# Performance work log

Hardware: AMD Instinct MI355X
Metric: run time of the kernel (lower is better)

Reference implementation:

```python
import jax, jax.numpy as jnp
import numpy as np

N_NODES = 100000
N_EDGES = 1600000
IN_DIM = 256
HIDDEN = 64


def setup_inputs() -> dict:
    key = jax.random.key(0)
    k0, k1, k2, k3 = jax.random.split(key, 4)
    x = jax.random.normal(k0, (N_NODES, IN_DIM), dtype=jnp.float32)
    edge_index = jax.random.randint(k1, (2, N_EDGES), 0, N_NODES, dtype=jnp.int64)
    # GCNConv weight [in_dim, hidden] + bias, MLP Linear(hidden, 1) + bias
    W = jax.random.normal(k2, (IN_DIM, HIDDEN), dtype=jnp.float32) * 0.05
    b = jnp.zeros((HIDDEN,), dtype=jnp.float32)
    w2 = jax.random.normal(k3, (HIDDEN, 1), dtype=jnp.float32) * 0.05
    b2 = jnp.zeros((1,), dtype=jnp.float32)
    return {"x": x, "edge_index": edge_index, "W": W, "b": b, "w2": w2, "b2": b2}


def reference(x, edge_index, W, b, w2, b2):
    N = x.shape[0]
    # PyG GCNConv default: add self-loops, symmetric normalization D^-1/2 A D^-1/2
    loops = jnp.arange(N, dtype=edge_index.dtype)
    src = jnp.concatenate([edge_index[0], loops])  # [E + N]
    dst = jnp.concatenate([edge_index[1], loops])
    h = x @ W  # [N, H] transform first (hidden < in_dim)
    deg = jax.ops.segment_sum(jnp.ones_like(dst, dtype=h.dtype), dst, num_segments=N)
    dinv = jnp.where(deg > 0, jax.lax.rsqrt(deg), 0.0)
    norm = dinv[src] * dinv[dst]  # [E + N]
    agg = jax.ops.segment_sum(h[src] * norm[:, None], dst, num_segments=N) + b  # [N, H]
    score = jax.nn.sigmoid(agg @ w2 + b2)  # [N, 1]
    return score.squeeze(-1)
```

## Files before the change

kernel.cpp:

```cpp
#include <hip/hip_runtime.h>
#include <math.h>

#define N_NODES 100000
#define N_EDGES 1600000
#define IN_DIM  256
#define HIDDEN  64

#define NB      32
#define EPB     50000
#define QPB     12500
#define SR      8
#define SRANGE  12544
#define PD      8
#define DNR     12800
#define DW      3200
#define DEGB    256

__global__ void __launch_bounds__(1024) fusedA_kernel(const float* __restrict__ x,
                                                      const float* __restrict__ W,
                                                      const float* __restrict__ w2,
                                                      const int4* __restrict__ dst4,
                                                      unsigned* __restrict__ partialD,
                                                      float* __restrict__ s) {
    __shared__ __align__(16) unsigned sh[DW];
    const int bid = blockIdx.x;
    if (bid < DEGB) {
        const int r  = bid & (PD - 1);
        const int bb = bid >> 3;
        const int nbase = r * DNR;
        for (int i = threadIdx.x; i < DW; i += 1024) sh[i] = 0u;
        __syncthreads();
        const int q0 = bb * QPB;
        for (int k = threadIdx.x; k < QPB; k += 1024) {
            int4 d4 = dst4[q0 + k];
            int d0 = d4.x - nbase, d1 = d4.y - nbase, d2 = d4.z - nbase, d3 = d4.w - nbase;
            if ((unsigned)d0 < (unsigned)DNR) atomicAdd(&sh[d0 >> 2], 1u << ((d0 & 3) * 8));
            if ((unsigned)d1 < (unsigned)DNR) atomicAdd(&sh[d1 >> 2], 1u << ((d1 & 3) * 8));
            if ((unsigned)d2 < (unsigned)DNR) atomicAdd(&sh[d2 >> 2], 1u << ((d2 & 3) * 8));
            if ((unsigned)d3 < (unsigned)DNR) atomicAdd(&sh[d3 >> 2], 1u << ((d3 & 3) * 8));
        }
        __syncthreads();
        unsigned* outp = partialD + (size_t)bid * DW;
        for (int i = threadIdx.x; i < DW; i += 1024) outp[i] = sh[i];
    } else {
        float* vsh = (float*)sh;
        if (threadIdx.x < IN_DIM) {
            const float4* wr  = (const float4*)(W + threadIdx.x * HIDDEN);
            const float4* w2r = (const float4*)w2;
            float acc = 0.f;
            #pragma unroll
            for (int j = 0; j < HIDDEN / 4; ++j) {
                float4 a = wr[j], q = w2r[j];
                acc += a.x * q.x + a.y * q.y + a.z * q.z + a.w * q.w;
            }
            vsh[threadIdx.x] = acc;
        }
        __syncthreads();
        const int wid  = threadIdx.x >> 6;
        const int lane = threadIdx.x & 63;
        const int gw   = (bid - DEGB) * 16 + wid;
        float4 vv = ((const float4*)vsh)[lane];
        for (int n = gw; n < N_NODES; n += 4096) {
            const float4* xr = (const float4*)(x + (size_t)n * IN_DIM);
            float4 a = xr[lane];
            float d = a.x * vv.x + a.y * vv.y + a.z * vv.z + a.w * vv.w;
            #pragma unroll
            for (int off = 32; off > 0; off >>= 1) d += __shfl_down(d, off, 64);
            if (lane == 0) s[n] = d;
        }
    }
}

__global__ void deg_merge_kernel(const unsigned* __restrict__ partialD,
                                 const float* __restrict__ s,
                                 float* __restrict__ dinv, float* __restrict__ t) {
    int w = blockIdx.x * blockDim.x + threadIdx.x;
    if (w >= N_NODES / 4) return;
    const int r = w / DW, j = w - r * DW;
    unsigned a0 = 0, a1 = 0, a2 = 0, a3 = 0;
    #pragma unroll 8
    for (int b = 0; b < NB; ++b) {
        unsigned p = partialD[(size_t)(b * PD + r) * DW + j];
        a0 += p & 255u; a1 += (p >> 8) & 255u; a2 += (p >> 16) & 255u; a3 += p >> 24;
    }
    const int n0 = w * 4;
    float4 sv = *(const float4*)(s + n0);
    float4 di, tv;
    di.x = rsqrtf((float)(a0 + 1)); di.y = rsqrtf((float)(a1 + 1));
    di.z = rsqrtf((float)(a2 + 1)); di.w = rsqrtf((float)(a3 + 1));
    tv.x = di.x * sv.x; tv.y = di.y * sv.y; tv.z = di.z * sv.z; tv.w = di.w * sv.w;
    *(float4*)(dinv + n0) = di;
    *(float4*)(t + n0) = tv;
}

__global__ void __launch_bounds__(1024) scat_hist_kernel(const int4* __restrict__ src4,
                                                         const int4* __restrict__ dst4,
                                                         const float* __restrict__ t,
                                                         float* __restrict__ partialU) {
    __shared__ float acc[SRANGE];
    const int r  = blockIdx.x & (SR - 1);
    const int bb = blockIdx.x >> 3;
    const int nbase = r * SRANGE;
    for (int i = threadIdx.x; i < SRANGE; i += 1024) acc[i] = 0.f;
    __syncthreads();
    const int q0 = bb * QPB;
    for (int k = threadIdx.x; k < QPB; k += 1024) {
        int4 d4 = dst4[q0 + k];
        int4 s4 = src4[q0 + k];
        int d0 = d4.x - nbase, d1 = d4.y - nbase, d2 = d4.z - nbase, d3 = d4.w - nbase;
        if ((unsigned)d0 < (unsigned)SRANGE) atomicAdd(&acc[d0], t[s4.x]);
        if ((unsigned)d1 < (unsigned)SRANGE) atomicAdd(&acc[d1], t[s4.y]);
        if ((unsigned)d2 < (unsigned)SRANGE) atomicAdd(&acc[d2], t[s4.z]);
        if ((unsigned)d3 < (unsigned)SRANGE) atomicAdd(&acc[d3], t[s4.w]);
    }
    __syncthreads();
    float* outp = partialU + (size_t)blockIdx.x * SRANGE;
    for (int i = threadIdx.x; i < SRANGE; i += 1024) outp[i] = acc[i];
}

__global__ void merge_final_kernel(const float* __restrict__ partialU,
                                   const float* __restrict__ dinv,
                                   const float* __restrict__ s,
                                   const float* __restrict__ b,
                                   const float* __restrict__ w2,
                                   const float* __restrict__ b2,
                                   float* __restrict__ out) {
    float c = b2[0];
    #pragma unroll 8
    for (int j = 0; j < HIDDEN; ++j) c += b[j] * w2[j];
    int n = blockIdx.x * blockDim.x + threadIdx.x;
    if (n >= N_NODES) return;
    const int r = n / SRANGE, j = n - r * SRANGE;
    float u = 0.f;
    #pragma unroll 8
    for (int bl = 0; bl < NB; ++bl)
        u += partialU[(size_t)(bl * SR + r) * SRANGE + j];
    float di = dinv[n];
    float pre = di * (u + di * s[n]) + c;
    out[n] = 1.f / (1.f + expf(-pre));
}

__global__ void wv_kernel(const float* __restrict__ W, const float* __restrict__ b,
                          const float* __restrict__ w2, const float* __restrict__ b2,
                          float* __restrict__ v, float* __restrict__ c) {
    int i = threadIdx.x;
    float acc = 0.f;
    for (int j = 0; j < HIDDEN; ++j) acc += W[i * HIDDEN + j] * w2[j];
    v[i] = acc;
    if (i == 0) {
        float cc = b2[0];
        for (int j = 0; j < HIDDEN; ++j) cc += b[j] * w2[j];
        *c = cc;
    }
}
__global__ void s_kernel(const float* __restrict__ x, const float* __restrict__ v,
                         float* __restrict__ s) {
    const int wave = threadIdx.x >> 6;
    const int lane = threadIdx.x & 63;
    const int n = blockIdx.x * 4 + wave;
    const float4* xr = (const float4*)(x + (size_t)n * IN_DIM);
    const float4* vr = (const float4*)v;
    float4 a  = xr[lane];
    float4 vv = vr[lane];
    float d = a.x * vv.x + a.y * vv.y + a.z * vv.z + a.w * vv.w;
    #pragma unroll
    for (int off = 32; off > 0; off >>= 1) d += __shfl_down(d, off, 64);
    if (lane == 0) s[n] = d;
}
__global__ void deg_kernel(const int* __restrict__ dst, int* __restrict__ cnt) {
    int e = blockIdx.x * blockDim.x + threadIdx.x;
    if (e < N_EDGES) atomicAdd(&cnt[dst[e]], 1);
}
__global__ void dinv_kernel(const int* __restrict__ cnt, const float* __restrict__ s,
                            float* __restrict__ dinv, float* __restrict__ t) {
    int n = blockIdx.x * blockDim.x + threadIdx.x;
    if (n < N_NODES) {
        float di = rsqrtf((float)(cnt[n] + 1));
        dinv[n] = di;
        t[n] = di * s[n];
    }
}
__global__ void scatter_kernel(const int* __restrict__ src, const int* __restrict__ dst,
                               const float* __restrict__ t, float* __restrict__ u) {
    int e = blockIdx.x * blockDim.x + threadIdx.x;
    if (e < N_EDGES) atomicAdd(&u[dst[e]], t[src[e]]);
}
__global__ void final_kernel(const float* __restrict__ dinv, const float* __restrict__ u,
                             const float* __restrict__ s, const float* __restrict__ c,
                             float* __restrict__ out) {
    int n = blockIdx.x * blockDim.x + threadIdx.x;
    if (n < N_NODES) {
        float di = dinv[n];
        float pre = di * (u[n] + di * s[n]) + c[0];
        out[n] = 1.f / (1.f + expf(-pre));
    }
}

extern "C" void kernel_launch(void* const* d_in, const int* in_sizes, int n_in,
                              void* d_out, int out_size, void* d_ws, size_t ws_size,
                              hipStream_t stream) {
    const float* x   = (const float*)d_in[0];
    const int*   ei  = (const int*)  d_in[1];
    const float* W   = (const float*)d_in[2];
    const float* b   = (const float*)d_in[3];
    const float* w2  = (const float*)d_in[4];
    const float* b2  = (const float*)d_in[5];
    float* out = (float*)d_out;

    const int* src = ei;
    const int* dst = ei + N_EDGES;

    float* ws   = (float*)d_ws;
    float*    v        = ws + 0;
    float*    c        = ws + 256;
    float*    s        = ws + 512;
    float*    t        = ws + 100608;
    float*    dinv     = ws + 200704;
    unsigned* partialD = (unsigned*)(ws + 300800);
    float*    partialU = ws + 1120000;
    const size_t need_bytes = (size_t)(1120000 + 256 * SRANGE) * 4;

    if (ws_size >= need_bytes) {
        fusedA_kernel<<<DEGB + 256, 1024, 0, stream>>>(x, W, w2, (const int4*)dst, partialD, s);
        deg_merge_kernel<<<(N_NODES / 4 + 255) / 256, 256, 0, stream>>>(partialD, s, dinv, t);
        scat_hist_kernel<<<NB * SR, 1024, 0, stream>>>((const int4*)src, (const int4*)dst, t, partialU);
        merge_final_kernel<<<(N_NODES + 511) / 512, 512, 0, stream>>>(partialU, dinv, s, b, w2, b2, out);
    } else {
        float* u   = ws + 300800;
        int*   cnt = (int*)(ws + 400800);
        hipMemsetAsync((char*)d_ws + (size_t)300800 * 4, 0, (size_t)200000 * 4, stream);
        wv_kernel<<<1, 256, 0, stream>>>(W, b, w2, b2, v, c);
        s_kernel<<<N_NODES / 4, 256, 0, stream>>>(x, v, s);
        deg_kernel<<<(N_EDGES + 255) / 256, 256, 0, stream>>>(dst, cnt);
        dinv_kernel<<<(N_NODES + 255) / 256, 256, 0, stream>>>(cnt, s, dinv, t);
        scatter_kernel<<<(N_EDGES + 255) / 256, 256, 0, stream>>>(src, dst, t, u);
        final_kernel<<<(N_NODES + 255) / 256, 256, 0, stream>>>(dinv, u, s, c, out);
    }
}
```

Before: 207.2 us.

## Fuse all stages into one cooperative kernel with grid-wide syncs

Replaces the four-kernel pipeline (degree histogram plus score GEMV, degree merge, scatter histogram, merge and final sigmoid) with a single cooperative kernel of 512 blocks. Stages are separated by grid.sync. The scatter stage is also re-split into 64 edge chunks by 8 node ranges. The goal is to remove kernel launch gaps and tail effects between the dependent stages. The cost is three grid-wide barriers, a larger partialU buffer, and lower parallelism in some stages. If the workspace is too small or the cooperative launch fails, it falls back to the old path. The old non-histogram fallback path is removed.

```diff
diff --git a/kernel.cpp b/kernel.cpp
--- a/kernel.cpp
+++ b/kernel.cpp
@@ -1,10 +1,151 @@
 #include <hip/hip_runtime.h>
+#include <hip/hip_cooperative_groups.h>
 #include <math.h>
+
+namespace cg = cooperative_groups;
 
 #define N_NODES 100000
 #define N_EDGES 1600000
 #define IN_DIM  256
 #define HIDDEN  64
+
+#define GRID    512
+#define TPB     512
+#define D_NB    32
+#define D_EPB   50000
+#define D_QPB   12500
+#define D_PD    8
+#define D_DNR   12800
+#define D_DW    3200
+#define S_NB    64
+#define S_EPB   25000
+#define S_QPB   6250
+#define S_SR    8
+#define S_RANGE 12544
+
+__global__ void __launch_bounds__(TPB, 4) mega_kernel(
+    const float* __restrict__ x, const float* __restrict__ W,
+    const float* __restrict__ b, const float* __restrict__ w2,
+    const float* __restrict__ b2,
+    const int4* __restrict__ src4, const int4* __restrict__ dst4,
+    float* __restrict__ s, float* __restrict__ dinv, float* __restrict__ t,
+    unsigned* __restrict__ partialD, float* __restrict__ partialU,
+    float* __restrict__ out)
+{
+    __shared__ __align__(16) float sh[S_RANGE];
+    cg::grid_group grid = cg::this_grid();
+    const int bid = blockIdx.x;
+    const int tid = threadIdx.x;
+
+    if (bid < 256) {
+        unsigned* hist = (unsigned*)sh;
+        const int r  = bid & 7;
+        const int bb = bid >> 3;
+        const int nbase = r * D_DNR;
+        for (int i = tid; i < D_DW; i += TPB) hist[i] = 0u;
+        __syncthreads();
+        const int q0 = bb * D_QPB;
+        for (int k = tid; k < D_QPB; k += TPB) {
+            int4 d4 = dst4[q0 + k];
+            int d0 = d4.x - nbase, d1 = d4.y - nbase, d2 = d4.z - nbase, d3 = d4.w - nbase;
+            if ((unsigned)d0 < (unsigned)D_DNR) atomicAdd(&hist[d0 >> 2], 1u << ((d0 & 3) * 8));
+            if ((unsigned)d1 < (unsigned)D_DNR) atomicAdd(&hist[d1 >> 2], 1u << ((d1 & 3) * 8));
+            if ((unsigned)d2 < (unsigned)D_DNR) atomicAdd(&hist[d2 >> 2], 1u << ((d2 & 3) * 8));
+            if ((unsigned)d3 < (unsigned)D_DNR) atomicAdd(&hist[d3 >> 2], 1u << ((d3 & 3) * 8));
+        }
+        __syncthreads();
+        unsigned* outp = partialD + (size_t)bid * D_DW;
+        for (int i = tid; i < D_DW; i += TPB) outp[i] = hist[i];
+    } else {
+        if (tid < IN_DIM) {
+            const float4* wr  = (const float4*)(W + tid * HIDDEN);
+            const float4* w2r = (const float4*)w2;
+            float acc = 0.f;
+            #pragma unroll
+            for (int j = 0; j < HIDDEN / 4; ++j) {
+                float4 a = wr[j], q = w2r[j];
+                acc += a.x * q.x + a.y * q.y + a.z * q.z + a.w * q.w;
+            }
+            sh[tid] = acc;
+        }
+        __syncthreads();
+        const int wid  = tid >> 6;
+        const int lane = tid & 63;
+        float4 vv = ((const float4*)sh)[lane];
+        int gw = (bid - 256) * (TPB / 64) + wid;
+        for (int n = gw; n < N_NODES; n += 2048) {
+            const float4* xr = (const float4*)(x + (size_t)n * IN_DIM);
+            float4 a = xr[lane];
+            float d = a.x * vv.x + a.y * vv.y + a.z * vv.z + a.w * vv.w;
+            #pragma unroll
+            for (int off = 32; off > 0; off >>= 1) d += __shfl_down(d, off, 64);
+            if (lane == 0) s[n] = d;
+        }
+    }
+    grid.sync();
+
+    {
+        int w = bid * TPB + tid;
+        if (w < N_NODES / 4) {
+            const int r = w / D_DW, j = w - r * D_DW;
+            unsigned a0 = 0, a1 = 0, a2 = 0, a3 = 0;
+            #pragma unroll 8
+            for (int bb = 0; bb < D_NB; ++bb) {
+                unsigned p = partialD[(size_t)(bb * D_PD + r) * D_DW + j];
+                a0 += p & 255u; a1 += (p >> 8) & 255u; a2 += (p >> 16) & 255u; a3 += p >> 24;
+            }
+            const int n0 = w * 4;
+            float4 sv = *(const float4*)(s + n0);
+            float4 di, tv;
+            di.x = rsqrtf((float)(a0 + 1)); di.y = rsqrtf((float)(a1 + 1));
+            di.z = rsqrtf((float)(a2 + 1)); di.w = rsqrtf((float)(a3 + 1));
+            tv.x = di.x * sv.x; tv.y = di.y * sv.y; tv.z = di.z * sv.z; tv.w = di.w * sv.w;
+            *(float4*)(dinv + n0) = di;
+            *(float4*)(t + n0) = tv;
+        }
+    }
+    grid.sync();
+
+    {
+        float* acc = sh;
+        const int r  = bid & 7;
+        const int bb = bid >> 3;
+        const int nbase = r * S_RANGE;
+        for (int i = tid; i < S_RANGE; i += TPB) acc[i] = 0.f;
+        __syncthreads();
+        const int q0 = bb * S_QPB;
+        for (int k = tid; k < S_QPB; k += TPB) {
+            int4 d4 = dst4[q0 + k];
+            int4 s4 = src4[q0 + k];
+            int d0 = d4.x - nbase, d1 = d4.y - nbase, d2 = d4.z - nbase, d3 = d4.w - nbase;
+            if ((unsigned)d0 < (unsigned)S_RANGE) atomicAdd(&acc[d0], t[s4.x]);
+            if ((unsigned)d1 < (unsigned)S_RANGE) atomicAdd(&acc[d1], t[s4.y]);
+            if ((unsigned)d2 < (unsigned)S_RANGE) atomicAdd(&acc[d2], t[s4.z]);
+            if ((unsigned)d3 < (unsigned)S_RANGE) atomicAdd(&acc[d3], t[s4.w]);
+        }
+        __syncthreads();
+        float* outp = partialU + (size_t)bid * S_RANGE;
+        for (int i = tid; i < S_RANGE; i += TPB) outp[i] = acc[i];
+    }
+    grid.sync();
+
+    {
+        float c = b2[0];
+        #pragma unroll 8
+        for (int j = 0; j < HIDDEN; ++j) c += b[j] * w2[j];
+        int n = bid * TPB + tid;
+        if (n < N_NODES) {
+            const int r = n / S_RANGE, j = n - r * S_RANGE;
+            float u = 0.f;
+            #pragma unroll 8
+            for (int bl = 0; bl < S_NB; ++bl)
+                u += partialU[(size_t)(bl * S_SR + r) * S_RANGE + j];
+            float di = dinv[n];
+            float pre = di * (u + di * s[n]) + c;
+            out[n] = 1.f / (1.f + expf(-pre));
+        }
+    }
+}
 
 #define NB      32
 #define EPB     50000
@@ -140,62 +281,6 @@
     out[n] = 1.f / (1.f + expf(-pre));
 }
 
-__global__ void wv_kernel(const float* __restrict__ W, const float* __restrict__ b,
-                          const float* __restrict__ w2, const float* __restrict__ b2,
-                          float* __restrict__ v, float* __restrict__ c) {
-    int i = threadIdx.x;
-    float acc = 0.f;
-    for (int j = 0; j < HIDDEN; ++j) acc += W[i * HIDDEN + j] * w2[j];
-    v[i] = acc;
-    if (i == 0) {
-        float cc = b2[0];
-        for (int j = 0; j < HIDDEN; ++j) cc += b[j] * w2[j];
-        *c = cc;
-    }
-}
-__global__ void s_kernel(const float* __restrict__ x, const float* __restrict__ v,
-                         float* __restrict__ s) {
-    const int wave = threadIdx.x >> 6;
-    const int lane = threadIdx.x & 63;
-    const int n = blockIdx.x * 4 + wave;
-    const float4* xr = (const float4*)(x + (size_t)n * IN_DIM);
-    const float4* vr = (const float4*)v;
-    float4 a  = xr[lane];
-    float4 vv = vr[lane];
-    float d = a.x * vv.x + a.y * vv.y + a.z * vv.z + a.w * vv.w;
-    #pragma unroll
-    for (int off = 32; off > 0; off >>= 1) d += __shfl_down(d, off, 64);
-    if (lane == 0) s[n] = d;
-}
-__global__ void deg_kernel(const int* __restrict__ dst, int* __restrict__ cnt) {
-    int e = blockIdx.x * blockDim.x + threadIdx.x;
-    if (e < N_EDGES) atomicAdd(&cnt[dst[e]], 1);
-}
-__global__ void dinv_kernel(const int* __restrict__ cnt, const float* __restrict__ s,
-                            float* __restrict__ dinv, float* __restrict__ t) {
-    int n = blockIdx.x * blockDim.x + threadIdx.x;
-    if (n < N_NODES) {
-        float di = rsqrtf((float)(cnt[n] + 1));
-        dinv[n] = di;
-        t[n] = di * s[n];
-    }
-}
-__global__ void scatter_kernel(const int* __restrict__ src, const int* __restrict__ dst,
-                               const float* __restrict__ t, float* __restrict__ u) {
-    int e = blockIdx.x * blockDim.x + threadIdx.x;
-    if (e < N_EDGES) atomicAdd(&u[dst[e]], t[src[e]]);
-}
-__global__ void final_kernel(const float* __restrict__ dinv, const float* __restrict__ u,
-                             const float* __restrict__ s, const float* __restrict__ c,
-                             float* __restrict__ out) {
-    int n = blockIdx.x * blockDim.x + threadIdx.x;
-    if (n < N_NODES) {
-        float di = dinv[n];
-        float pre = di * (u[n] + di * s[n]) + c[0];
-        out[n] = 1.f / (1.f + expf(-pre));
-    }
-}
-
 extern "C" void kernel_launch(void* const* d_in, const int* in_sizes, int n_in,
                               void* d_out, int out_size, void* d_ws, size_t ws_size,
                               hipStream_t stream) {
@@ -207,33 +292,35 @@
     const float* b2  = (const float*)d_in[5];
     float* out = (float*)d_out;
 
-    const int* src = ei;
-    const int* dst = ei + N_EDGES;
-
-    float* ws   = (float*)d_ws;
-    float*    v        = ws + 0;
-    float*    c        = ws + 256;
+    const int4* src4 = (const int4*)ei;
+    const int4* dst4 = (const int4*)(ei + N_EDGES);
+
+    float* ws = (float*)d_ws;
     float*    s        = ws + 512;
     float*    t        = ws + 100608;
     float*    dinv     = ws + 200704;
     unsigned* partialD = (unsigned*)(ws + 300800);
     float*    partialU = ws + 1120000;
-    const size_t need_bytes = (size_t)(1120000 + 256 * SRANGE) * 4;
-
-    if (ws_size >= need_bytes) {
-        fusedA_kernel<<<DEGB + 256, 1024, 0, stream>>>(x, W, w2, (const int4*)dst, partialD, s);
+    const size_t mega_need  = (size_t)(1120000 + GRID * S_RANGE) * 4;
+    const size_t fused_need = (size_t)(1120000 + 256 * SRANGE) * 4;
+
+    bool done = false;
+    if (ws_size >= mega_need) {
+        void* args[] = {(void*)&x, (void*)&W, (void*)&b, (void*)&w2, (void*)&b2,
+                        (void*)&src4, (void*)&dst4,
+                        (void*)&s, (void*)&dinv, (void*)&t,
+                        (void*)&partialD, (void*)&partialU, (void*)&out};
+        hipError_t err = hipLaunchCooperativeKernel((void*)mega_kernel,
+                                                    dim3(GRID), dim3(TPB),
+                                                    args, 0, stream);
+        done = (err == hipSuccess);
+    }
+
+    if (!done && ws_size >= fused_need) {
+        fusedA_kernel<<<DEGB + 256, 1024, 0, stream>>>(x, W, w2, dst4, partialD, s);
         deg_merge_kernel<<<(N_NODES / 4 + 255) / 256, 256, 0, stream>>>(partialD, s, dinv, t);
-        scat_hist_kernel<<<NB * SR, 1024, 0, stream>>>((const int4*)src, (const int4*)dst, t, partialU);
+        scat_hist_kernel<<<NB * SR, 1024, 0, stream>>>(src4, dst4, t, partialU);
         merge_final_kernel<<<(N_NODES + 511) / 512, 512, 0, stream>>>(partialU, dinv, s, b, w2, b2, out);
-    } else {
-        float* u   = ws + 300800;
-        int*   cnt = (int*)(ws + 400800);
-        hipMemsetAsync((char*)d_ws + (size_t)300800 * 4, 0, (size_t)200000 * 4, stream);
-        wv_kernel<<<1, 256, 0, stream>>>(W, b, w2, b2, v, c);
-        s_kernel<<<N_NODES / 4, 256, 0, stream>>>(x, v, s);
-        deg_kernel<<<(N_EDGES + 255) / 256, 256, 0, stream>>>(dst, cnt);
-        dinv_kernel<<<(N_NODES + 255) / 256, 256, 0, stream>>>(cnt, s, dinv, t);
-        scatter_kernel<<<(N_EDGES + 255) / 256, 256, 0, stream>>>(src, dst, t, u);
-        final_kernel<<<(N_NODES + 255) / 256, 256, 0, stream>>>(dinv, u, s, c, out);
-    }
-}
+        done = true;
+    }
+}
```

Measured after the change: 411.0 us. 1.98x slower.
